# Kernel optimization log

Measured on AMD Instinct MI355X. Metric: run time of the kernel, lower is better.

Reference implementation:

```python
import jax, jax.numpy as jnp
import numpy as np

B, C, H, T, K = 32, 128, 512, 8192, 512


def setup_inputs() -> dict:
    key = jax.random.key(0)
    ks = jax.random.split(key, 4)
    s = 0.02
    return {
        "x": jax.random.normal(ks[0], (B, C, T), dtype=jnp.float32),
        "up_w": jax.random.normal(ks[1], (H, C), dtype=jnp.float32) * s,
        "up_b": jnp.zeros((H,), jnp.float32),
        "sal_w": jax.random.normal(ks[2], (H, C), dtype=jnp.float32) * s,
        "sal_b": jnp.zeros((H,), jnp.float32),
        "down_w": jax.random.normal(ks[3], (C, H), dtype=jnp.float32) * s,
        "down_b": jnp.zeros((C,), jnp.float32),
        "k_sparse": K,
    }


def reference(x, up_w, up_b, sal_w, sal_b, down_w, down_b, k_sparse):
    b = x.shape[0]
    # 1x1 Conv1d == per-timestep GEMM
    sig = jnp.einsum('bct,hc->bht', x, up_w) + up_b[None, :, None]   # [B,H,T]
    sal = jnp.einsum('bct,hc->bht', x, sal_w) + sal_b[None, :, None]  # [B,H,T]
    # global softmax over flattened (H*T) per batch item
    flat = jax.nn.softmax(sal.reshape(b, -1), axis=-1)                # [B,H*T]
    # k-sparse: keep top-k values, zero everything else
    vals, idx = jax.lax.top_k(flat, k_sparse)                          # [B,K]
    sparse = jnp.zeros_like(flat).at[jnp.arange(b)[:, None], idx].set(vals)
    sal_sparse = sparse.reshape(sig.shape)                             # [B,H,T]
    gated = sig * sal_sparse                                           # [B,H,T]
    out = jnp.einsum('bht,ch->bct', gated, down_w) + down_b[None, :, None]
    return out
```

## Files before the change

### kernel.cpp

```cpp
#include <hip/hip_runtime.h>
#include <hip/hip_bf16.h>
#include <math.h>

#define BB 32
#define CC 128
#define HH 512
#define TT 8192
#define KMAX 512

#define NBIN 2048
#define CANDCAP 4096
#define HOTCAP 32768
#define TILES 2048
#define TLCAP 256
#define HFLOOR 0.6f
#define BW (0.875f / 2048.0f)
#define INVBW (2048.0f / 0.875f)
#define DELTA_C2 6e-3f
#define DELTA_C1 1.2e-2f

#define N_HIST 0
#define N_SUMEXP 262144
#define N_CANDCNT 262400
#define N_TILECNT 262528
#define N_ZERO 270720
#define N_TAU 270848
#define N_SELCNT 270976
#define N_CELLMAX 271360
#define N_TLIST 8659968
#define N_CANDVAL 10757120
#define N_CANDIDX 11805696
#define N_SELIDX 12329984
#define N_SELVAL 12395520
#define N_SWB 12461056
#define N_XF 12592128
#define N_DWT 79700992
#define N_NEED 79963136

#define O_HIST 0
#define O_SUMEXP 262144
#define O_CANDCNT 262400
#define O_HOTCNT 262528
#define O_ZERO 262656
#define O_TAU 262656
#define O_SELCNT 262784
#define O_CELLMAX 263168
#define O_HOTLIST 8651776
#define O_CANDVAL 8782848
#define O_CANDIDX 9831424
#define O_SELIDX 10355712
#define O_SELVAL 10421248

typedef __attribute__((ext_vector_type(8))) short short8;
typedef __attribute__((ext_vector_type(16))) float f32x16;
typedef __attribute__((address_space(3))) unsigned int lds_u32;
typedef const __attribute__((address_space(1))) unsigned int glb_u32;


__global__ void prep_w(const float* __restrict__ sw, short* __restrict__ swb) {
  int i = blockIdx.x * 256 + threadIdx.x;
  int m = i & 31, u = (i >> 5) & 1, kc = (i >> 6) & 7, w = (i >> 9) & 3, by = i >> 11;
  int h = by * 128 + w * 32 + m;
  int c0 = kc * 16 + u * 8;
  float4 f0 = *(const float4*)(sw + (size_t)h * CC + c0);
  float4 f1 = *(const float4*)(sw + (size_t)h * CC + c0 + 4);
  union { __hip_bfloat162 h2; unsigned u; } p0, p1, p2, p3;
  p0.h2 = __float22bfloat162_rn(make_float2(f0.x, f0.y));
  p1.h2 = __float22bfloat162_rn(make_float2(f0.z, f0.w));
  p2.h2 = __float22bfloat162_rn(make_float2(f1.x, f1.y));
  p3.h2 = __float22bfloat162_rn(make_float2(f1.z, f1.w));
  *(uint4*)(swb + (size_t)i * 8) = make_uint4(p0.u, p1.u, p2.u, p3.u);
}

__global__ void prep_dwt(const float* __restrict__ dw, float* __restrict__ dwt) {
  int i = blockIdx.x * 256 + threadIdx.x;
  int c = i & 127, h = i >> 7;
  dwt[(size_t)h * CC + c] = dw[(size_t)c * HH + h];
}

__global__ __launch_bounds__(256) void prep_xt(const float* __restrict__ x,
                                               short* __restrict__ xf) {
  __shared__ float Lt[128 * 128];
  int tid = threadIdx.x;
  int b = blockIdx.y, bx = blockIdx.x, t0g = bx * 128;
  const float* xb = x + (size_t)b * CC * TT;
  {
    int cq = tid >> 5, tq = tid & 31, t0 = tq * 4;
#pragma unroll
    for (int p = 0; p < 4; p++) {
      int c0 = p * 32 + cq * 4;
      float r0[4], r1[4], r2[4], r3[4];
      *(float4*)r0 = *(const float4*)(xb + (size_t)(c0 + 0) * TT + t0g + t0);
      *(float4*)r1 = *(const float4*)(xb + (size_t)(c0 + 1) * TT + t0g + t0);
      *(float4*)r2 = *(const float4*)(xb + (size_t)(c0 + 2) * TT + t0g + t0);
      *(float4*)r3 = *(const float4*)(xb + (size_t)(c0 + 3) * TT + t0g + t0);
#pragma unroll
      for (int j = 0; j < 4; j++) {
        int t = t0 + j;
        int addr = t * 128 + ((((c0 >> 2) ^ (t & 31)) << 2));
        *(float4*)&Lt[addr] = make_float4(r0[j], r1[j], r2[j], r3[j]);
      }
    }
  }
  __syncthreads();
  int u = tid & 1, m = (tid >> 1) & 31, nt = (tid >> 6) & 3;
  int t = nt * 32 + m;
  short* dst = xf + ((size_t)b * 64 + bx) * 16384 + nt * 4096 + u * 256 + m * 8;
#pragma unroll
  for (int kc = 0; kc < 8; kc++) {
    int c0 = kc * 16 + u * 8;
    float4 f0 = *(float4*)&Lt[t * 128 + ((((c0 >> 2) ^ (t & 31)) << 2))];
    float4 f1 = *(float4*)&Lt[t * 128 + (((((c0 + 4) >> 2) ^ (t & 31)) << 2))];
    union { __hip_bfloat162 h2; unsigned u; } p0, p1, p2, p3;
    p0.h2 = __float22bfloat162_rn(make_float2(f0.x, f0.y));
    p1.h2 = __float22bfloat162_rn(make_float2(f0.z, f0.w));
    p2.h2 = __float22bfloat162_rn(make_float2(f1.x, f1.y));
    p3.h2 = __float22bfloat162_rn(make_float2(f1.z, f1.w));
    *(uint4*)(dst + kc * 512) = make_uint4(p0.u, p1.u, p2.u, p3.u);
  }
}

__global__ __launch_bounds__(256) void pass_a_lds(const short* __restrict__ xf,
                                                  const short* __restrict__ swb,
                                                  const float* __restrict__ sb,
                                                  float* __restrict__ cellmax,
                                                  int* __restrict__ hist,
                                                  double* __restrict__ sumexp) {
  __shared__ short Xs[16384];
  __shared__ double sered[4];
  int tid = threadIdx.x;
  int w = tid >> 6, lane = tid & 63, m = lane & 31, u = lane >> 5;
  int id = blockIdx.x, b = blockIdx.y;
  int bx = ((id >> 5) << 3) | (id & 7);
  int by = (id >> 3) & 3;

  const short* xsl = xf + ((size_t)b * 64 + bx) * 16384;
  {
    const short* gs = xsl + w * 4096 + lane * 8;
    short* ls = &Xs[w * 4096];
#pragma unroll
    for (int i = 0; i < 8; i++) {
      __builtin_amdgcn_global_load_lds((glb_u32*)(gs + i * 512),
                                       (lds_u32*)(ls + i * 512), 16, 0, 0);
    }
  }

  const short* wb_ = swb + (size_t)(by * 4 + w) * 4096 + u * 256 + m * 8;
  short8 afr[8];
#pragma unroll
  for (int kc = 0; kc < 8; kc++) afr[kc] = *(const short8*)(wb_ + kc * 512);

  __syncthreads();

  f32x16 acc0, acc1, acc2, acc3;
#pragma unroll
  for (int r = 0; r < 16; r++) { acc0[r] = 0.f; acc1[r] = 0.f; acc2[r] = 0.f; acc3[r] = 0.f; }

  const short* xr = &Xs[u * 256 + m * 8];
#pragma unroll
  for (int kc = 0; kc < 8; kc++) {
    short8 b0 = *(const short8*)(xr + kc * 512);
    short8 b1 = *(const short8*)(xr + 4096 + kc * 512);
    short8 b2 = *(const short8*)(xr + 8192 + kc * 512);
    short8 b3 = *(const short8*)(xr + 12288 + kc * 512);
    acc0 = __builtin_amdgcn_mfma_f32_32x32x16_bf16(afr[kc], b0, acc0, 0, 0, 0);
    acc1 = __builtin_amdgcn_mfma_f32_32x32x16_bf16(afr[kc], b1, acc1, 0, 0, 0);
    acc2 = __builtin_amdgcn_mfma_f32_32x32x16_bf16(afr[kc], b2, acc2, 0, 0, 0);
    acc3 = __builtin_amdgcn_mfma_f32_32x32x16_bf16(afr[kc], b3, acc3, 0, 0, 0);
  }

  int h0 = by * 128;
  float tmax = -1e30f;
  float se = 0.f;
#define EPI(ACC)                                                              \
  {                                                                           \
    _Pragma("unroll") for (int g = 0; g < 4; g++) {                           \
      float bias4[4];                                                         \
      *(float4*)bias4 = *(const float4*)&sb[h0 + w * 32 + g * 8 + u * 4];     \
      _Pragma("unroll") for (int q = 0; q < 4; q++) {                         \
        float s = ACC[g * 4 + q] + bias4[q];                                  \
        tmax = fmaxf(tmax, s);                                                \
        se += __expf(s);                                                      \
        if (s >= HFLOOR) {                                                    \
          int bin = (int)((s - HFLOOR) * INVBW);                              \
          if (bin > NBIN - 1) bin = NBIN - 1;                                 \
          atomicAdd(&hist[b * NBIN + bin], 1);                                \
        }                                                                     \
      }                                                                       \
    }                                                                         \
  }
  EPI(acc0) EPI(acc1) EPI(acc2) EPI(acc3)
#undef EPI
  int cid = ((b * 4 + by) * 64 + bx) * 256 + tid;
  cellmax[cid] = tmax;
  double sed = (double)se;
#pragma unroll
  for (int mm = 1; mm < 64; mm <<= 1) sed += __shfl_xor(sed, mm);
  if (lane == 0) sered[w] = sed;
  __syncthreads();
  if (tid == 0) atomicAdd(&sumexp[b], sered[0] + sered[1] + sered[2] + sered[3]);
}

__global__ void pass_b(const int* __restrict__ hist, float* __restrict__ tau,
                       const int* __restrict__ kptr) {
  __shared__ int hsh[NBIN];
  __shared__ int ps[256];
  int b = blockIdx.x, tid = threadIdx.x;
  int part = 0;
#pragma unroll
  for (int j = 0; j < 8; j++) {
    int v = hist[b * NBIN + tid * 8 + j];
    hsh[tid * 8 + j] = v;
    part += v;
  }
  ps[tid] = part;
  __syncthreads();
  if (tid == 0) {
    int k = kptr[0];
    if (k < 1) k = 1;
    if (k > KMAX) k = KMAX;
    long cum = 0;
    float tv = HFLOOR;
    for (int i = 255; i >= 0; i--) {
      if (cum + ps[i] >= k) {
        long r = k - cum;
        long c2 = 0;
        for (int j = 7; j >= 0; j--) {
          c2 += hsh[i * 8 + j];
          if (c2 >= r) { tv = HFLOOR + (i * 8 + j) * BW; break; }
        }
        break;
      }
      cum += ps[i];
    }
    tau[b] = tv;
  }
}

__global__ void pass_c1_fast(const float* __restrict__ cellmax, const float* __restrict__ tau,
                             int* __restrict__ tilecnt, int* __restrict__ tlist) {
  int i = blockIdx.x * blockDim.x + threadIdx.x;
  float v = cellmax[i];
  int b = i >> 16;
  if (v >= tau[b] - DELTA_C1) {
    int tile = (b << 6) | ((i >> 8) & 63);
    int pos = atomicAdd(&tilecnt[tile], 1);
    if (pos < TLCAP) tlist[tile * TLCAP + pos] = i;
  }
}

__global__ __launch_bounds__(512) void pass_c2_fast(
    const float* __restrict__ x, const float* __restrict__ sw,
    const float* __restrict__ sb, const float* __restrict__ tau,
    const int* __restrict__ tilecnt, const int* __restrict__ tlist,
    int* __restrict__ candcnt, double* __restrict__ candval, int* __restrict__ candidx) {
  __shared__ float Xt[128 * 132];
  __shared__ float4 Wsh[8 * 512];
  int tile = blockIdx.x;
  int b = tile >> 6, bx = tile & 63;
  int cnt = tilecnt[tile];
  if (cnt <= 0) return;
  if (cnt > TLCAP) cnt = TLCAP;
  int tid = threadIdx.x;
  {
    int cq = tid >> 5, tq = tid & 31, t4 = tq * 4;
    int sw4 = ((t4 >> 5) & 3) << 2;
    const float* xb = x + (size_t)b * CC * TT + bx * 128;
#pragma unroll
    for (int p = 0; p < 8; p++) {
      int c = p * 16 + cq;
      float4 v = *(const float4*)(xb + (size_t)c * TT + t4);
      int cc = c ^ sw4;
      Xt[(t4 + 0) * 132 + cc] = v.x;
      Xt[(t4 + 1) * 132 + cc] = v.y;
      Xt[(t4 + 2) * 132 + cc] = v.z;
      Xt[(t4 + 3) * 132 + cc] = v.w;
    }
  }
  __syncthreads();
  int wv = tid >> 6, lane = tid & 63;
  if (wv >= cnt) return;
  int nt = lane >> 4, r = lane & 15;
  int rs = r & 7;
  int rowp = lane >> 5, colp = lane & 31;
  float tmb = tau[b] - DELTA_C2;
  int tbase = tile * TLCAP;
  float4* WbF4 = &Wsh[wv * 512];

  int s = wv;
  int cid = tlist[tbase + s];
  for (; s < cnt;) {
    int by_ = (cid >> 14) & 3, ta_ = cid & 255;
    int w_ = ta_ >> 6, lc_ = ta_ & 63, m_ = lc_ & 31, u_ = lc_ >> 5;
    int hbase = by_ * 128 + w_ * 32 + 4 * u_;
    int h = hbase + (r >> 2) * 8 + (r & 3);
    int t = bx * 128 + nt * 32 + m_;
    const float* xrp = &Xt[(nt * 32 + m_) * 132];
#pragma unroll
    for (int i = 0; i < 8; i++) {
      int row_ = i * 2 + rowp;
      int h_ = hbase + ((row_ >> 2) << 3) + (row_ & 3);
      int c4 = colp ^ (row_ & 7);
      __builtin_amdgcn_global_load_lds(
          (glb_u32*)(sw + (size_t)h_ * CC + c4 * 4),
          (lds_u32*)((char*)WbF4 + i * 1024), 16, 0, 0);
    }
    float sbh = sb[h];
    int sn = s + 8;
    int cidN = (sn < cnt) ? tlist[tbase + sn] : 0;
    asm volatile("s_waitcnt vmcnt(0)" ::: "memory");
    __builtin_amdgcn_sched_barrier(0);
    double a0 = 0.0, a1 = 0.0, a2 = 0.0, a3 = 0.0;
#pragma unroll
    for (int j = 0; j < 32; j++) {
      float4 w4 = WbF4[r * 32 + (j ^ rs)];
      float4 x4 = *(const float4*)(xrp + ((j * 4) ^ (nt * 4)));
      a0 = fma((double)x4.x, (double)w4.x, a0);
      a1 = fma((double)x4.y, (double)w4.y, a1);
      a2 = fma((double)x4.z, (double)w4.z, a2);
      a3 = fma((double)x4.w, (double)w4.w, a3);
    }
    double acc = a0 + a1 + a2 + a3 + (double)sbh;
    if (acc >= (double)tmb) {
      int pos = atomicAdd(&candcnt[b], 1);
      if (pos < CANDCAP) {
        candval[b * CANDCAP + pos] = acc;
        candidx[b * CANDCAP + pos] = h * TT + t;
      }
    }
    s = sn;
    cid = cidN;
  }
}

__global__ void pass_d(const int* __restrict__ candcnt, const double* __restrict__ candval,
                       const int* __restrict__ candidx, const double* __restrict__ sumexp,
                       const int* __restrict__ kptr, int* __restrict__ selidx,
                       float* __restrict__ selval, int* __restrict__ selcnt) {
  __shared__ double sv[CANDCAP];
  __shared__ int si[CANDCAP];
  int b = blockIdx.x;
  int n = candcnt[b];
  if (n > CANDCAP) n = CANDCAP;
  int k = kptr[0];
  if (k < 0) k = 0;
  if (k > KMAX) k = KMAX;
  for (int i = threadIdx.x; i < n; i += blockDim.x) {
    sv[i] = candval[b * CANDCAP + i];
    si[i] = candidx[b * CANDCAP + i];
  }
  __syncthreads();
  double S = sumexp[b];
  for (int i = threadIdx.x; i < n; i += blockDim.x) {
    double vi = sv[i];
    int ii = si[i];
    int rank = 0;
    for (int q = 0; q < n; q++) {
      double vq = sv[q];
      rank += (vq > vi) || (vq == vi && si[q] < ii);
    }
    if (rank < k) {
      selidx[b * KMAX + rank] = ii;
      selval[b * KMAX + rank] = (float)(exp(vi) / S);
    }
  }
  if (threadIdx.x == 0) selcnt[b] = n < k ? n : k;
}

__global__ void pass_e1(const float* __restrict__ db, float* __restrict__ out) {
  int row = blockIdx.x;
  int c = row & (CC - 1);
  float v = db[c];
  float4 v4 = make_float4(v, v, v, v);
  float4* o = (float4*)(out + (size_t)row * TT);
#pragma unroll
  for (int q = 0; q < 8; q++) o[q * 256 + threadIdx.x] = v4;
}

__global__ void pass_e2_fast(const short* __restrict__ xf, const float* __restrict__ uw,
                             const float* __restrict__ ub, const float* __restrict__ dwt,
                             const int* __restrict__ selidx, const float* __restrict__ selval,
                             const int* __restrict__ selcnt, float* __restrict__ out) {
  int b = blockIdx.y, j = blockIdx.x;
  if (j >= selcnt[b]) return;
  int idx = selidx[b * KMAX + j];
  float val = selval[b * KMAX + j];
  int h = idx >> 13, t = idx & (TT - 1);
  int bx = t >> 7, tl = t & 127, nt = tl >> 5, m = tl & 31;
  int lane = threadIdx.x;
  const short* xt = xf + ((size_t)b * 64 + bx) * 16384 + nt * 4096 + m * 8;
  int off = (lane >> 3) * 512 + ((lane >> 2) & 1) * 256 + (lane & 3) * 2;
  __hip_bfloat162 hv = *(const __hip_bfloat162*)(xt + off);
  float2 xv = __bfloat1622float2(hv);
  int c0 = lane * 2;
  float2 wv = *(const float2*)(uw + (size_t)h * CC + c0);
  float p = xv.x * wv.x + xv.y * wv.y;
#pragma unroll
  for (int mm = 1; mm < 64; mm <<= 1) p += __shfl_xor(p, mm);
  float sig = p + ub[h];
  float g = sig * val;
  float2 dv = *(const float2*)(dwt + (size_t)h * CC + c0);
  atomicAdd(&out[((size_t)b * CC + c0) * TT + t], g * dv.x);
  atomicAdd(&out[((size_t)b * CC + c0 + 1) * TT + t], g * dv.y);
}

__global__ __launch_bounds__(256) void pass_a_slow(const float* __restrict__ x,
                                                   const float* __restrict__ sw,
                                                   const float* __restrict__ sb,
                                                   float* __restrict__ cellmax,
                                                   int* __restrict__ hist,
                                                   double* __restrict__ sumexp) {
  __shared__ short Ws[128 * 128];
  __shared__ short Xs[128 * 128];
  __shared__ float sbs[128];
  int tid = threadIdx.x;
  int b = blockIdx.z, by = blockIdx.y, bx = blockIdx.x;
  int h0 = by * 128, t0g = bx * 128;
  const float* xb = x + (size_t)b * CC * TT;
  {
    int cq = tid >> 5, tq = tid & 31;
    int t0 = tq * 4;
#pragma unroll
    for (int p = 0; p < 4; p++) {
      int c0 = p * 32 + cq * 4;
      float r0[4], r1[4], r2[4], r3[4];
      *(float4*)r0 = *(const float4*)(xb + (size_t)(c0 + 0) * TT + t0g + t0);
      *(float4*)r1 = *(const float4*)(xb + (size_t)(c0 + 1) * TT + t0g + t0);
      *(float4*)r2 = *(const float4*)(xb + (size_t)(c0 + 2) * TT + t0g + t0);
      *(float4*)r3 = *(const float4*)(xb + (size_t)(c0 + 3) * TT + t0g + t0);
#pragma unroll
      for (int j = 0; j < 4; j++) {
        int t = t0 + j;
        int addr = t * 128 + ((((c0 >> 3) ^ (t & 15)) << 3) | (c0 & 7));
        union { __hip_bfloat162 h; unsigned int u; } a0, a1;
        a0.h = __float22bfloat162_rn(make_float2(r0[j], r1[j]));
        a1.h = __float22bfloat162_rn(make_float2(r2[j], r3[j]));
        *(uint2*)&Xs[addr] = make_uint2(a0.u, a1.u);
      }
    }
  }
  {
    int hh = tid >> 1, c4 = (tid & 1) << 2;
#pragma unroll
    for (int k = 0; k < 16; k++) {
      int c0 = k * 8 + c4;
      float r[4];
      *(float4*)r = *(const float4*)(sw + (size_t)(h0 + hh) * CC + c0);
      int addr = hh * 128 + ((((c0 >> 3) ^ (hh & 15)) << 3) | (c0 & 7));
      union { __hip_bfloat162 h; unsigned int u; } a0, a1;
      a0.h = __float22bfloat162_rn(make_float2(r[0], r[1]));
      a1.h = __float22bfloat162_rn(make_float2(r[2], r[3]));
      *(uint2*)&Ws[addr] = make_uint2(a0.u, a1.u);
    }
  }
  if (tid < 128) sbs[tid] = sb[h0 + tid];
  __syncthreads();
  int w = tid >> 6, lane = tid & 63, m = lane & 31, u = lane >> 5;
  f32x16 acc0, acc1, acc2, acc3;
#pragma unroll
  for (int r = 0; r < 16; r++) { acc0[r] = 0.f; acc1[r] = 0.f; acc2[r] = 0.f; acc3[r] = 0.f; }
  const short* wrow = &Ws[(w * 32 + m) * 128];
  const short* xrow = &Xs[m * 128];
#pragma unroll
  for (int kc = 0; kc < 8; kc++) {
    int pc = ((((kc << 1) | u) ^ (m & 15)) << 3);
    short8 af = *(const short8*)(wrow + pc);
    short8 b0 = *(const short8*)(xrow + 0 * 32 * 128 + pc);
    short8 b1 = *(const short8*)(xrow + 1 * 32 * 128 + pc);
    short8 b2 = *(const short8*)(xrow + 2 * 32 * 128 + pc);
    short8 b3 = *(const short8*)(xrow + 3 * 32 * 128 + pc);
    acc0 = __builtin_amdgcn_mfma_f32_32x32x16_bf16(af, b0, acc0, 0, 0, 0);
    acc1 = __builtin_amdgcn_mfma_f32_32x32x16_bf16(af, b1, acc1, 0, 0, 0);
    acc2 = __builtin_amdgcn_mfma_f32_32x32x16_bf16(af, b2, acc2, 0, 0, 0);
    acc3 = __builtin_amdgcn_mfma_f32_32x32x16_bf16(af, b3, acc3, 0, 0, 0);
  }
  float tmax = -1e30f;
  float se = 0.f;
#define EPI(ACC)                                                              \
  {                                                                           \
    _Pragma("unroll") for (int g = 0; g < 4; g++) {                           \
      float bias4[4];                                                         \
      *(float4*)bias4 = *(float4*)&sbs[w * 32 + g * 8 + u * 4];               \
      _Pragma("unroll") for (int q = 0; q < 4; q++) {                         \
        float s = ACC[g * 4 + q] + bias4[q];                                  \
        tmax = fmaxf(tmax, s);                                                \
        se += __expf(s);                                                      \
        if (s >= HFLOOR) {                                                    \
          int bin = (int)((s - HFLOOR) * INVBW);                              \
          if (bin > NBIN - 1) bin = NBIN - 1;                                 \
          atomicAdd(&hist[b * NBIN + bin], 1);                                \
        }                                                                     \
      }                                                                       \
    }                                                                         \
  }
  EPI(acc0) EPI(acc1) EPI(acc2) EPI(acc3)
#undef EPI
  int cid = ((b * 4 + by) * 64 + bx) * 256 + tid;
  cellmax[cid] = tmax;
  double sed = (double)se;
#pragma unroll
  for (int mm = 1; mm < 64; mm <<= 1) sed += __shfl_xor(sed, mm);
  if ((tid & 63) == 0) atomicAdd(&sumexp[b], sed);
}

__global__ void pass_c1_slow(const float* __restrict__ cellmax, const float* __restrict__ tau,
                             int* __restrict__ hotcnt, int* __restrict__ hotlist) {
  int i = blockIdx.x * blockDim.x + threadIdx.x;
  float v = cellmax[i];
  int b = i >> 16;
  if (v >= tau[b] - DELTA_C1) {
    int pos = atomicAdd(hotcnt, 1);
    if (pos < HOTCAP) hotlist[pos] = i;
  }
}

__global__ void pass_c2_slow(const float* __restrict__ x, const float* __restrict__ sw,
                             const float* __restrict__ sb, const float* __restrict__ tau,
                             const int* __restrict__ hotcnt, const int* __restrict__ hotlist,
                             int* __restrict__ candcnt, double* __restrict__ candval,
                             int* __restrict__ candidx) {
  int j = blockIdx.x;
  int n = hotcnt[0];
  if (n > HOTCAP) n = HOTCAP;
  if (j >= n) return;
  int cid = hotlist[j];
  int b = cid >> 16, by = (cid >> 14) & 3, bx = (cid >> 8) & 63;
  int ta = cid & 255;
  int w = ta >> 6, lane = ta & 63, m = lane & 31, u = lane >> 5;
  int e = threadIdx.x;
  int nt = e >> 4, r = e & 15;
  int h = by * 128 + w * 32 + (r >> 2) * 8 + (r & 3) + 4 * u;
  int t = bx * 128 + nt * 32 + m;
  const float* xb = x + (size_t)b * CC * TT;
  double acc = 0.0;
#pragma unroll 8
  for (int c = 0; c < CC; c++)
    acc += (double)xb[(size_t)c * TT + t] * (double)sw[h * CC + c];
  acc += (double)sb[h];
  float tm = tau[b] - DELTA_C2;
  if (acc >= (double)tm) {
    int pos = atomicAdd(&candcnt[b], 1);
    if (pos < CANDCAP) {
      candval[b * CANDCAP + pos] = acc;
      candidx[b * CANDCAP + pos] = h * TT + t;
    }
  }
}

__global__ void pass_e2_slow(const float* __restrict__ x, const float* __restrict__ uw,
                             const float* __restrict__ ub, const float* __restrict__ dw,
                             const int* __restrict__ selidx, const float* __restrict__ selval,
                             const int* __restrict__ selcnt, float* __restrict__ out) {
  int b = blockIdx.y, j = blockIdx.x;
  if (j >= selcnt[b]) return;
  int idx = selidx[b * KMAX + j];
  float val = selval[b * KMAX + j];
  int h = idx >> 13, t = idx & (TT - 1);
  int c = threadIdx.x;
  const float* xb = x + (size_t)b * CC * TT;
  float p = xb[(size_t)c * TT + t] * uw[h * CC + c] +
            xb[(size_t)(c + 64) * TT + t] * uw[h * CC + c + 64];
#pragma unroll
  for (int m = 1; m < 64; m <<= 1) p += __shfl_xor(p, m);
  float sig = p + ub[h];
  float g = sig * val;
  atomicAdd(&out[((size_t)b * CC + c) * TT + t], g * dw[c * HH + h]);
  atomicAdd(&out[((size_t)b * CC + c + 64) * TT + t], g * dw[(c + 64) * HH + h]);
}

extern "C" void kernel_launch(void* const* d_in, const int* in_sizes, int n_in,
                              void* d_out, int out_size, void* d_ws, size_t ws_size,
                              hipStream_t stream) {
  const float* x = (const float*)d_in[0];
  const float* uw = (const float*)d_in[1];
  const float* ub = (const float*)d_in[2];
  const float* sw = (const float*)d_in[3];
  const float* sb = (const float*)d_in[4];
  const float* dw = (const float*)d_in[5];
  const float* db = (const float*)d_in[6];
  const int* kptr = (const int*)d_in[7];
  float* out = (float*)d_out;
  char* ws = (char*)d_ws;

  if (ws_size >= (size_t)N_NEED) {
    int* hist = (int*)(ws + N_HIST);
    double* sumexp = (double*)(ws + N_SUMEXP);
    int* candcnt = (int*)(ws + N_CANDCNT);
    int* tilecnt = (int*)(ws + N_TILECNT);
    float* tau = (float*)(ws + N_TAU);
    int* selcnt = (int*)(ws + N_SELCNT);
    float* cellmax = (float*)(ws + N_CELLMAX);
    int* tlist = (int*)(ws + N_TLIST);
    double* candval = (double*)(ws + N_CANDVAL);
    int* candidx = (int*)(ws + N_CANDIDX);
    int* selidx = (int*)(ws + N_SELIDX);
    float* selval = (float*)(ws + N_SELVAL);
    short* swb = (short*)(ws + N_SWB);
    short* xf = (short*)(ws + N_XF);
    float* dwt = (float*)(ws + N_DWT);

    (void)hipMemsetAsync(d_ws, 0, N_ZERO, stream);
    prep_w<<<32, 256, 0, stream>>>(sw, swb);
    prep_dwt<<<256, 256, 0, stream>>>(dw, dwt);
    prep_xt<<<dim3(64, 32), 256, 0, stream>>>(x, xf);
    pass_a_lds<<<dim3(256, 32), 256, 0, stream>>>(xf, swb, sb, cellmax, hist, sumexp);
    pass_b<<<32, 256, 0, stream>>>(hist, tau, kptr);
    pass_c1_fast<<<8192, 256, 0, stream>>>(cellmax, tau, tilecnt, tlist);
    pass_c2_fast<<<TILES, 512, 0, stream>>>(x, sw, sb, tau, tilecnt, tlist, candcnt,
                                            candval, candidx);
    pass_d<<<32, 256, 0, stream>>>(candcnt, candval, candidx, sumexp, kptr, selidx,
                                   selval, selcnt);
    pass_e1<<<BB * CC, 256, 0, stream>>>(db, out);
    pass_e2_fast<<<dim3(KMAX, BB), 64, 0, stream>>>(xf, uw, ub, dwt, selidx, selval,
                                                    selcnt, out);
  } else {
    int* hist = (int*)(ws + O_HIST);
    double* sumexp = (double*)(ws + O_SUMEXP);
    int* candcnt = (int*)(ws + O_CANDCNT);
    int* hotcnt = (int*)(ws + O_HOTCNT);
    float* tau = (float*)(ws + O_TAU);
    int* selcnt = (int*)(ws + O_SELCNT);
    float* cellmax = (float*)(ws + O_CELLMAX);
    int* hotlist = (int*)(ws + O_HOTLIST);
    double* candval = (double*)(ws + O_CANDVAL);
    int* candidx = (int*)(ws + O_CANDIDX);
    int* selidx = (int*)(ws + O_SELIDX);
    float* selval = (float*)(ws + O_SELVAL);

    (void)hipMemsetAsync(d_ws, 0, O_ZERO, stream);
    pass_a_slow<<<dim3(64, 4, 32), 256, 0, stream>>>(x, sw, sb, cellmax, hist, sumexp);
    pass_b<<<32, 256, 0, stream>>>(hist, tau, kptr);
    pass_c1_slow<<<8192, 256, 0, stream>>>(cellmax, tau, hotcnt, hotlist);
    pass_c2_slow<<<HOTCAP, 64, 0, stream>>>(x, sw, sb, tau, hotcnt, hotlist, candcnt,
                                            candval, candidx);
    pass_d<<<32, 256, 0, stream>>>(candcnt, candval, candidx, sumexp, kptr, selidx,
                                   selval, selcnt);
    pass_e1<<<BB * CC, 256, 0, stream>>>(db, out);
    pass_e2_slow<<<dim3(KMAX, BB), 64, 0, stream>>>(x, uw, ub, dw, selidx, selval,
                                                    selcnt, out);
  }
}
```

Baseline: 923.1 us.

## Replace per-tile hot-cell lists with flat global list and one wave per cell

The candidate-rescoring pass no longer groups hot cells by time tile with a 128x128 x-tile staged in LDS. Instead the first pass appends hot cells to a single global list, and the second pass launches one 64-thread block per list entry that loads only the needed x columns directly. This is meant to remove the large per-tile x staging and the idle waves in sparsely populated tiles. In exchange it launches HOTCAP blocks, most of which exit early, and funnels every append through one global atomic counter.

```diff
diff --git a/kernel.cpp b/kernel.cpp
--- a/kernel.cpp
+++ b/kernel.cpp
@@ -238,98 +238,77 @@
 }
 
 __global__ void pass_c1_fast(const float* __restrict__ cellmax, const float* __restrict__ tau,
-                             int* __restrict__ tilecnt, int* __restrict__ tlist) {
+                             int* __restrict__ hotcnt, int* __restrict__ hotlist) {
   int i = blockIdx.x * blockDim.x + threadIdx.x;
   float v = cellmax[i];
   int b = i >> 16;
   if (v >= tau[b] - DELTA_C1) {
-    int tile = (b << 6) | ((i >> 8) & 63);
-    int pos = atomicAdd(&tilecnt[tile], 1);
-    if (pos < TLCAP) tlist[tile * TLCAP + pos] = i;
-  }
-}
-
-__global__ __launch_bounds__(512) void pass_c2_fast(
+    int pos = atomicAdd(hotcnt, 1);
+    if (pos < HOTCAP) hotlist[pos] = i;
+  }
+}
+
+__global__ __launch_bounds__(64) void pass_c2_fast(
     const float* __restrict__ x, const float* __restrict__ sw,
     const float* __restrict__ sb, const float* __restrict__ tau,
-    const int* __restrict__ tilecnt, const int* __restrict__ tlist,
+    const int* __restrict__ hotcnt, const int* __restrict__ hotlist,
     int* __restrict__ candcnt, double* __restrict__ candval, int* __restrict__ candidx) {
-  __shared__ float Xt[128 * 132];
-  __shared__ float4 Wsh[8 * 512];
-  int tile = blockIdx.x;
-  int b = tile >> 6, bx = tile & 63;
-  int cnt = tilecnt[tile];
-  if (cnt <= 0) return;
-  if (cnt > TLCAP) cnt = TLCAP;
-  int tid = threadIdx.x;
-  {
-    int cq = tid >> 5, tq = tid & 31, t4 = tq * 4;
-    int sw4 = ((t4 >> 5) & 3) << 2;
-    const float* xb = x + (size_t)b * CC * TT + bx * 128;
-#pragma unroll
-    for (int p = 0; p < 8; p++) {
-      int c = p * 16 + cq;
-      float4 v = *(const float4*)(xb + (size_t)c * TT + t4);
-      int cc = c ^ sw4;
-      Xt[(t4 + 0) * 132 + cc] = v.x;
-      Xt[(t4 + 1) * 132 + cc] = v.y;
-      Xt[(t4 + 2) * 132 + cc] = v.z;
-      Xt[(t4 + 3) * 132 + cc] = v.w;
-    }
-  }
-  __syncthreads();
-  int wv = tid >> 6, lane = tid & 63;
-  if (wv >= cnt) return;
-  int nt = lane >> 4, r = lane & 15;
-  int rs = r & 7;
+  __shared__ float Xc[4 * 132];
+  __shared__ float4 Wp[16 * 32];
+  int j = blockIdx.x;
+  int n = hotcnt[0];
+  if (n > HOTCAP) n = HOTCAP;
+  if (j >= n) return;
+  int cid = hotlist[j];
+  int b = cid >> 16, by = (cid >> 14) & 3, bx = (cid >> 8) & 63;
+  int ta = cid & 255;
+  int w_ = ta >> 6, lc = ta & 63, m_ = lc & 31, u_ = lc >> 5;
+  int lane = threadIdx.x;
+  int nt = lane >> 4, r = lane & 15, rs = r & 7;
+  int hbase = by * 128 + w_ * 32 + 4 * u_;
+  int h = hbase + (r >> 2) * 8 + (r & 3);
+  int t = bx * 128 + nt * 32 + m_;
+  const float* xb = x + (size_t)b * CC * TT;
+
+  float xv[8];
+#pragma unroll
+  for (int p = 0; p < 8; p++) xv[p] = xb[(size_t)(p * 16 + r) * TT + t];
+
   int rowp = lane >> 5, colp = lane & 31;
+#pragma unroll
+  for (int i2 = 0; i2 < 8; i2++) {
+    int row_ = i2 * 2 + rowp;
+    int h_ = hbase + ((row_ >> 2) << 3) + (row_ & 3);
+    int c4 = colp ^ (row_ & 7);
+    __builtin_amdgcn_global_load_lds((glb_u32*)(sw + (size_t)h_ * CC + c4 * 4),
+                                     (lds_u32*)((char*)Wp + i2 * 1024), 16, 0, 0);
+  }
+  float sbh = sb[h];
   float tmb = tau[b] - DELTA_C2;
-  int tbase = tile * TLCAP;
-  float4* WbF4 = &Wsh[wv * 512];
-
-  int s = wv;
-  int cid = tlist[tbase + s];
-  for (; s < cnt;) {
-    int by_ = (cid >> 14) & 3, ta_ = cid & 255;
-    int w_ = ta_ >> 6, lc_ = ta_ & 63, m_ = lc_ & 31, u_ = lc_ >> 5;
-    int hbase = by_ * 128 + w_ * 32 + 4 * u_;
-    int h = hbase + (r >> 2) * 8 + (r & 3);
-    int t = bx * 128 + nt * 32 + m_;
-    const float* xrp = &Xt[(nt * 32 + m_) * 132];
-#pragma unroll
-    for (int i = 0; i < 8; i++) {
-      int row_ = i * 2 + rowp;
-      int h_ = hbase + ((row_ >> 2) << 3) + (row_ & 3);
-      int c4 = colp ^ (row_ & 7);
-      __builtin_amdgcn_global_load_lds(
-          (glb_u32*)(sw + (size_t)h_ * CC + c4 * 4),
-          (lds_u32*)((char*)WbF4 + i * 1024), 16, 0, 0);
-    }
-    float sbh = sb[h];
-    int sn = s + 8;
-    int cidN = (sn < cnt) ? tlist[tbase + sn] : 0;
-    asm volatile("s_waitcnt vmcnt(0)" ::: "memory");
-    __builtin_amdgcn_sched_barrier(0);
-    double a0 = 0.0, a1 = 0.0, a2 = 0.0, a3 = 0.0;
-#pragma unroll
-    for (int j = 0; j < 32; j++) {
-      float4 w4 = WbF4[r * 32 + (j ^ rs)];
-      float4 x4 = *(const float4*)(xrp + ((j * 4) ^ (nt * 4)));
-      a0 = fma((double)x4.x, (double)w4.x, a0);
-      a1 = fma((double)x4.y, (double)w4.y, a1);
-      a2 = fma((double)x4.z, (double)w4.z, a2);
-      a3 = fma((double)x4.w, (double)w4.w, a3);
-    }
-    double acc = a0 + a1 + a2 + a3 + (double)sbh;
-    if (acc >= (double)tmb) {
-      int pos = atomicAdd(&candcnt[b], 1);
-      if (pos < CANDCAP) {
-        candval[b * CANDCAP + pos] = acc;
-        candidx[b * CANDCAP + pos] = h * TT + t;
-      }
-    }
-    s = sn;
-    cid = cidN;
+  asm volatile("s_waitcnt vmcnt(0)" ::: "memory");
+#pragma unroll
+  for (int p = 0; p < 8; p++) Xc[nt * 132 + p * 16 + r] = xv[p];
+  asm volatile("s_waitcnt lgkmcnt(0)" ::: "memory");
+  __builtin_amdgcn_sched_barrier(0);
+
+  double a0 = 0.0, a1 = 0.0, a2 = 0.0, a3 = 0.0;
+  const float* xrp = &Xc[nt * 132];
+#pragma unroll
+  for (int jj = 0; jj < 32; jj++) {
+    float4 w4 = Wp[r * 32 + (jj ^ rs)];
+    float4 x4 = *(const float4*)(xrp + jj * 4);
+    a0 = fma((double)x4.x, (double)w4.x, a0);
+    a1 = fma((double)x4.y, (double)w4.y, a1);
+    a2 = fma((double)x4.z, (double)w4.z, a2);
+    a3 = fma((double)x4.w, (double)w4.w, a3);
+  }
+  double acc = a0 + a1 + a2 + a3 + (double)sbh;
+  if (acc >= (double)tmb) {
+    int pos = atomicAdd(&candcnt[b], 1);
+    if (pos < CANDCAP) {
+      candval[b * CANDCAP + pos] = acc;
+      candidx[b * CANDCAP + pos] = h * TT + t;
+    }
   }
 }
 
@@ -586,11 +565,11 @@
     int* hist = (int*)(ws + N_HIST);
     double* sumexp = (double*)(ws + N_SUMEXP);
     int* candcnt = (int*)(ws + N_CANDCNT);
-    int* tilecnt = (int*)(ws + N_TILECNT);
+    int* hotcnt = (int*)(ws + N_TILECNT);
     float* tau = (float*)(ws + N_TAU);
     int* selcnt = (int*)(ws + N_SELCNT);
     float* cellmax = (float*)(ws + N_CELLMAX);
-    int* tlist = (int*)(ws + N_TLIST);
+    int* hotlist = (int*)(ws + N_TLIST);
     double* candval = (double*)(ws + N_CANDVAL);
     int* candidx = (int*)(ws + N_CANDIDX);
     int* selidx = (int*)(ws + N_SELIDX);
@@ -605,8 +584,8 @@
     prep_xt<<<dim3(64, 32), 256, 0, stream>>>(x, xf);
     pass_a_lds<<<dim3(256, 32), 256, 0, stream>>>(xf, swb, sb, cellmax, hist, sumexp);
     pass_b<<<32, 256, 0, stream>>>(hist, tau, kptr);
-    pass_c1_fast<<<8192, 256, 0, stream>>>(cellmax, tau, tilecnt, tlist);
-    pass_c2_fast<<<TILES, 512, 0, stream>>>(x, sw, sb, tau, tilecnt, tlist, candcnt,
+    pass_c1_fast<<<8192, 256, 0, stream>>>(cellmax, tau, hotcnt, hotlist);
+    pass_c2_fast<<<HOTCAP, 64, 0, stream>>>(x, sw, sb, tau, hotcnt, hotlist, candcnt,
                                             candval, candidx);
     pass_d<<<32, 256, 0, stream>>>(candcnt, candval, candidx, sumexp, kptr, selidx,
                                    selval, selcnt);
```

New measurement: 1.106 ms. 1.2x slower.
